# Optimization experiments

Hardware: AMD Instinct MI355X
Metric: run time of the kernel (lower is better)

The kernel has to match this reference:

```python
import math
import jax, jax.numpy as jnp
import numpy as np

B, S, H, NH, BS, R = 2, 4096, 1024, 16, 64, 3
HD = H // NH          # 64 head dim
L = S // BS           # 64 blocks
PEN = -10000.0


def _make_rand_attn():
    # data-independent random block plan (like HF bigbird, seeded numpy),
    # per head, per middle query block: R random key blocks excluding
    # global blocks (0, L-1) and the sliding window (i-1, i, i+1)
    rng = np.random.RandomState(42)
    ra = np.zeros((NH, L - 2, R), dtype=np.int64)
    for h in range(NH):
        for i in range(1, L - 1):
            choices = np.array([j for j in range(L) if j not in (0, i - 1, i, i + 1, L - 1)])
            ra[h, i - 1] = rng.choice(choices, R, replace=False)
    return ra


def setup_inputs():
    key = jax.random.key(0)
    ks = jax.random.split(key, 8)
    sc = 1.0 / math.sqrt(H)
    return {
        "Q": jax.random.normal(ks[0], (B, S, H), jnp.float32),
        "K": jax.random.normal(ks[1], (B, S, H), jnp.float32),
        "V": jax.random.normal(ks[2], (B, S, H), jnp.float32),
        "mask": jnp.ones((B, S), jnp.float32),
        "Wq": jax.random.normal(ks[3], (H, H), jnp.float32) * sc,
        "bq": jnp.zeros((H,), jnp.float32),
        "Wk": jax.random.normal(ks[4], (H, H), jnp.float32) * sc,
        "bk": jnp.zeros((H,), jnp.float32),
        "Wv": jax.random.normal(ks[5], (H, H), jnp.float32) * sc,
        "bv": jnp.zeros((H,), jnp.float32),
        "rand_attn": jnp.asarray(_make_rand_attn()),
    }


def _forward(Q, K, V, mask, Wq, bq, Wk, bk, Wv, bv, rand_attn):
    rsd = 1.0 / math.sqrt(HD)
    sm = lambda x: jax.nn.softmax(x, axis=-1)

    def proj(x, W, b):  # torch Linear: x @ W^T + b, then split heads
        return (x @ W.T + b).reshape(B, S, NH, HD).transpose(0, 2, 1, 3)

    q = proj(Q, Wq, bq)  # [B,NH,S,HD]
    k = proj(K, Wk, bk)
    v = proj(V, Wv, bv)
    qb = q.reshape(B, NH, L, BS, HD)
    kb = k.reshape(B, NH, L, BS, HD)
    vb = v.reshape(B, NH, L, BS, HD)

    # ---- masks (derived from padding mask, as in HF create_masks_...) ----
    blocked = mask.reshape(B, L, BS)
    from_mask = mask[:, None, :, None]   # [B,1,S,1]
    to_mask = mask[:, None, None, :]     # [B,1,1,S]
    exp_to = jnp.concatenate([blocked[:, 1:-3], blocked[:, 2:-2], blocked[:, 3:-1]], axis=2)  # [B,L-4,3BS]
    band_mask = jnp.einsum('blq,blk->blqk', blocked[:, 2:-2], exp_to)[:, None]  # [B,1,L-4,BS,3BS]

    ra = jnp.broadcast_to(rand_attn[None], (B, NH, L - 2, R))
    bidx = jnp.arange(B)[:, None, None, None]
    hidx = jnp.arange(NH)[None, :, None, None]
    gk = kb[bidx, hidx, ra].reshape(B, NH, L - 2, R * BS, HD)  # gathered random key blocks
    gv = vb[bidx, hidx, ra].reshape(B, NH, L - 2, R * BS, HD)
    rm = blocked[bidx, ra].reshape(B, NH, L - 2, R * BS)
    rand_mask = jnp.einsum('blq,bhlk->bhlqk', blocked[:, 1:-1], rm)  # [B,NH,L-2,BS,R*BS]

    # ---- first block: dense attention over all keys ----
    p1 = jnp.einsum('bhqd,bhkd->bhqk', qb[:, :, 0], k) * rsd + (1.0 - to_mask) * PEN
    ctx_first = jnp.einsum('bhqk,bhkd->bhqd', sm(p1), v)

    # ---- second block: global(0) + window(1,2) + last + random ----
    k2 = jnp.concatenate([kb[:, :, 0], kb[:, :, 1], kb[:, :, 2], kb[:, :, -1], gk[:, :, 0]], axis=2)
    v2 = jnp.concatenate([vb[:, :, 0], vb[:, :, 1], vb[:, :, 2], vb[:, :, -1], gv[:, :, 0]], axis=2)
    p2 = jnp.einsum('bhqd,bhkd->bhqk', qb[:, :, 1], k2) * rsd
    seq_pad2 = jnp.concatenate([to_mask[..., :3 * BS], to_mask[..., -BS:],
                                jnp.ones((B, 1, 1, R * BS), mask.dtype)], axis=3)
    rand_pad2 = jnp.concatenate([jnp.ones((B, NH, BS, 4 * BS), mask.dtype), rand_mask[:, :, 0]], axis=3)
    p2 = p2 + (1.0 - jnp.minimum(seq_pad2, rand_pad2)) * PEN
    ctx_second = jnp.einsum('bhqk,bhkd->bhqd', sm(p2), v2)

    # ---- middle blocks: band (3 sliding) + random + 2 global ----
    exp_k = jnp.concatenate([kb[:, :, 1:-3], kb[:, :, 2:-2], kb[:, :, 3:-1]], axis=3)  # [B,NH,L-4,3BS,HD]
    exp_v = jnp.concatenate([vb[:, :, 1:-3], vb[:, :, 2:-2], vb[:, :, 3:-1]], axis=3)
    mq = qb[:, :, 2:-2]
    inner = jnp.einsum('bhlqd,bhlkd->bhlqk', mq, exp_k) * rsd + (1.0 - band_mask) * PEN
    randp = jnp.einsum('bhlqd,bhlkd->bhlqk', mq, gk[:, :, 1:-1]) * rsd + (1.0 - rand_mask[:, :, 1:-1]) * PEN
    firstp = jnp.einsum('bhlqd,bhkd->bhlqk', mq, kb[:, :, 0]) * rsd + (1.0 - to_mask[:, :, :, None, :BS]) * PEN
    lastp = jnp.einsum('bhlqd,bhkd->bhlqk', mq, kb[:, :, -1]) * rsd + (1.0 - to_mask[:, :, :, None, -BS:]) * PEN
    w = sm(jnp.concatenate([firstp, inner, randp, lastp], axis=-1))  # [B,NH,L-4,BS,(5+R)*BS]
    ctx_mid = jnp.einsum('bhlqk,bhlkd->bhlqd', w[..., BS:4 * BS], exp_v)
    ctx_mid += jnp.einsum('bhlqk,bhlkd->bhlqd', w[..., 4 * BS:(4 + R) * BS], gv[:, :, 1:-1])
    ctx_mid += jnp.einsum('bhlqk,bhkd->bhlqd', w[..., :BS], vb[:, :, 0])
    ctx_mid += jnp.einsum('bhlqk,bhkd->bhlqd', w[..., -BS:], vb[:, :, -1])

    # ---- second-to-last block ----
    k3 = jnp.concatenate([kb[:, :, 0], kb[:, :, -3], kb[:, :, -2], kb[:, :, -1], gk[:, :, -1]], axis=2)
    v3 = jnp.concatenate([vb[:, :, 0], vb[:, :, -3], vb[:, :, -2], vb[:, :, -1], gv[:, :, -1]], axis=2)
    p3 = jnp.einsum('bhqd,bhkd->bhqk', qb[:, :, -2], k3) * rsd
    seq_pad3 = jnp.concatenate([to_mask[..., :BS], to_mask[..., -3 * BS:],
                                jnp.ones((B, 1, 1, R * BS), mask.dtype)], axis=3)
    rand_pad3 = jnp.concatenate([jnp.ones((B, NH, BS, 4 * BS), mask.dtype), rand_mask[:, :, -1]], axis=3)
    p3 = p3 + (1.0 - jnp.minimum(seq_pad3, rand_pad3)) * PEN
    ctx_seclast = jnp.einsum('bhqk,bhkd->bhqd', sm(p3), v3)

    # ---- last block: dense attention over all keys ----
    p4 = jnp.einsum('bhqd,bhkd->bhqk', qb[:, :, -1], k) * rsd + (1.0 - to_mask) * PEN
    ctx_last = jnp.einsum('bhqk,bhkd->bhqd', sm(p4), v)

    ctx = jnp.concatenate([ctx_first[:, :, None], ctx_second[:, :, None], ctx_mid,
                           ctx_seclast[:, :, None], ctx_last[:, :, None]], axis=2)
    ctx = ctx.reshape(B, NH, S, HD) * from_mask
    return ctx.transpose(0, 2, 1, 3).reshape(B, S, NH * HD)


def reference(Q, K, V, mask, Wq, bq, Wk, bk, Wv, bv, rand_attn):
    return _forward(Q, K, V, mask, Wq, bq, Wk, bk, Wv, bv, rand_attn)
```

## Files before the change

### kernel.cpp

```cpp
#include <hip/hip_runtime.h>
#include <hip/hip_bf16.h>
#include <stdint.h>

#define BB 2
#define SS 4096
#define HH 1024
#define NHh 16
#define HD 64
#define LL 64
#define BS 64
#define RR 3
#define PENf (-10000.0f)
#define L2E 1.44269504f
#define PENL (-14426.9504f)

typedef unsigned int uint;
typedef __attribute__((ext_vector_type(8))) short bf16x8;
typedef __attribute__((ext_vector_type(4))) float f32x4;

__device__ __forceinline__ ushort f2bf(float f) {
    union { float f; uint u; } v; v.f = f;
    uint u = v.u;
    return (ushort)((u + 0x7fffu + ((u >> 16) & 1u)) >> 16);
}
__device__ __forceinline__ uint pack_bf(float a, float b) {
    uint r;
    asm("v_cvt_pk_bf16_f32 %0, %1, %2" : "=v"(r) : "v"(a), "v"(b));
    return r;
}
__device__ __forceinline__ float fexp2(float x) {
    float r;
    asm("v_exp_f32 %0, %1" : "=v"(r) : "v"(x));
    return r;
}
__device__ __forceinline__ float fmax3(float a, float b, float c) {
    float r;
    asm("v_max3_f32 %0, %1, %2, %3" : "=v"(r) : "v"(a), "v"(b), "v"(c));
    return r;
}
__device__ __forceinline__ uint scale_pair(uint w) {
    float lo = __uint_as_float(w << 16) * 0.125f;
    float hi = __uint_as_float(w & 0xffff0000u) * 0.125f;
    return pack_bf(lo, hi);
}
__device__ __forceinline__ uint4 scale4(uint4 w) {
    uint4 o;
    o.x = scale_pair(w.x); o.y = scale_pair(w.y);
    o.z = scale_pair(w.z); o.w = scale_pair(w.w);
    return o;
}
__device__ __forceinline__ void async16(const ushort* g, ushort* l) {
    __builtin_amdgcn_global_load_lds((const __attribute__((address_space(1))) uint*)g,
                                     (__attribute__((address_space(3))) uint*)l,
                                     16, 0, 0);
}

__global__ __launch_bounds__(256)
void cvt_kernel(const float* __restrict__ Xq, const float* __restrict__ Xk,
                const float* __restrict__ Xv, const float* __restrict__ Wq,
                const float* __restrict__ Wk, const float* __restrict__ Wv,
                ushort* __restrict__ Xbf, ushort* __restrict__ Wbf)
{
    const size_t XTOT = (size_t)3 * BB * SS * HH;
    const uint u = blockIdx.x * 256 + threadIdx.x;
    const size_t e = (size_t)u * 8;
    const float* src; ushort* dst;
    if (e < XTOT) {
        const int zz = (int)(e >> 23);
        src = (zz == 0 ? Xq : zz == 1 ? Xk : Xv) + (e & ((1u << 23) - 1));
        dst = Xbf + e;
    } else {
        const size_t e2 = e - XTOT;
        const int zz = (int)(e2 >> 20);
        src = (zz == 0 ? Wq : zz == 1 ? Wk : Wv) + (e2 & ((1u << 20) - 1));
        dst = Wbf + e2;
    }
    float4 a = ((const float4*)src)[0];
    float4 c = ((const float4*)src)[1];
    uint4 o;
    o.x = pack_bf(a.x, a.y); o.y = pack_bf(a.z, a.w);
    o.z = pack_bf(c.x, c.y); o.w = pack_bf(c.z, c.w);
    *(uint4*)dst = o;
}

__global__ __launch_bounds__(512)
void gemm6_kernel(const ushort* __restrict__ Xbf, const ushort* __restrict__ Wbf,
                  const float* __restrict__ bq, const float* __restrict__ bk,
                  const float* __restrict__ bv,
                  ushort* __restrict__ qb, ushort* __restrict__ kb,
                  ushort* __restrict__ vbT)
{
    __shared__ __align__(16) ushort smem6[36864];

    const int z = blockIdx.z;
    const ushort* Ag = Xbf + (size_t)z * ((size_t)BB * SS * HH);
    const ushort* Bg = Wbf + (size_t)z * (HH * HH);
    const float* bias = (z == 0) ? bq : (z == 1) ? bk : bv;
    const bool zv = (z == 2);

    const int tid = threadIdx.x;
    const int m0 = blockIdx.x * 128;
    const int n0 = blockIdx.y * 256;
    const int wave = tid >> 6;
    const int lane = tid & 63;
    const int l15 = lane & 15;
    const int quad = lane >> 4;
    const int wr = wave >> 2;
    const int wc = wave & 3;

    f32x4 acc[4][4];
#pragma unroll
    for (int i = 0; i < 4; ++i)
#pragma unroll
        for (int j = 0; j < 4; ++j) acc[i][j] = (f32x4){0.f, 0.f, 0.f, 0.f};

    const int trow = tid >> 2;
    const int tcol = ((tid & 3) ^ ((tid >> 3) & 3)) * 8;
    const ushort* Ath  = Ag + (size_t)(m0 + trow) * HH + tcol;
    const ushort* Bth  = Bg + (size_t)(n0 + trow) * HH + tcol;
    const ushort* Bth2 = Bth + (size_t)128 * HH;
    const int sl8 = (quad ^ ((l15 >> 1) & 3)) * 8;

#define STAGE6(kt_, bb_)                                               \
    do {                                                               \
        const int k0_ = (kt_) * 32;                                    \
        const int sb_ = (bb_) * 12288 + wave * 512;                    \
        async16(Ath + k0_,  smem6 + sb_);                              \
        async16(Bth + k0_,  smem6 + sb_ + 4096);                       \
        async16(Bth2 + k0_, smem6 + sb_ + 8192);                       \
    } while (0)

#define TB6(kt_, bpi_, VM_, DOSTAGE_, sbf_)                                         \
    do {                                                                            \
        const int bo_ = (bpi_) * 12288;                                             \
        asm volatile("s_waitcnt vmcnt(" #VM_ ")" ::: "memory");                     \
        __builtin_amdgcn_s_barrier();                                               \
        __builtin_amdgcn_sched_barrier(0);                                          \
        const ushort* Ab_ = smem6 + bo_;                                            \
        const ushort* Bb_ = smem6 + bo_ + 4096;                                     \
        bf16x8 af_[4], bf_[4];                                                      \
        _Pragma("unroll")                                                           \
        for (int mt = 0; mt < 4; ++mt)                                              \
            af_[mt] = *(const bf16x8*)(Ab_ + (wr * 64 + mt * 16 + l15) * 32 + sl8); \
        _Pragma("unroll")                                                           \
        for (int nt = 0; nt < 4; ++nt)                                              \
            bf_[nt] = *(const bf16x8*)(Bb_ + (wc * 64 + nt * 16 + l15) * 32 + sl8); \
        if (DOSTAGE_) STAGE6((kt_) + 2, sbf_);                                      \
        __builtin_amdgcn_s_setprio(1);                                              \
        if (zv) {                                                                   \
            _Pragma("unroll")                                                       \
            for (int i = 0; i < 4; ++i)                                             \
                _Pragma("unroll")                                                   \
                for (int j = 0; j < 4; ++j)                                         \
                    acc[i][j] = __builtin_amdgcn_mfma_f32_16x16x32_bf16(            \
                        af_[i], bf_[j], acc[i][j], 0, 0, 0);                        \
        } else {                                                                    \
            _Pragma("unroll")                                                       \
            for (int i = 0; i < 4; ++i)                                             \
                _Pragma("unroll")                                                   \
                for (int j = 0; j < 4; ++j)                                         \
                    acc[i][j] = __builtin_amdgcn_mfma_f32_16x16x32_bf16(            \
                        bf_[i], af_[j], acc[i][j], 0, 0, 0);                        \
        }                                                                           \
        __builtin_amdgcn_s_setprio(0);                                              \
    } while (0)

    STAGE6(0, 0); STAGE6(1, 1);

    for (int k3 = 0; k3 < 30; k3 += 3) {
        TB6(k3 + 0, 0, 3, 1, 2);
        TB6(k3 + 1, 1, 3, 1, 0);
        TB6(k3 + 2, 2, 3, 1, 1);
    }
    TB6(30, 0, 3, 0, 0);
    TB6(31, 1, 0, 0, 0);
#undef TB6
#undef STAGE6

    if (!zv) {
        ushort* outp = (z == 0) ? qb : kb;
#pragma unroll
        for (int wt = 0; wt < 4; ++wt) {
            const int nb = n0 + wc * 64 + wt * 16 + quad * 4;
            const float4 b4 = *(const float4*)&bias[nb];
            const int nh = nb >> 6;
            const int hd = nb & 63;
#pragma unroll
            for (int xt = 0; xt < 4; ++xt) {
                const int m = m0 + wr * 64 + xt * 16 + l15;
                const int bgl = m >> 12, s = m & 4095;
                uint2 pk;
                pk.x = pack_bf(acc[wt][xt][0] + b4.x, acc[wt][xt][1] + b4.y);
                pk.y = pack_bf(acc[wt][xt][2] + b4.z, acc[wt][xt][3] + b4.w);
                *(uint2*)&outp[((size_t)((bgl << 4) | nh) * SS + s) * HD + hd] = pk;
            }
        }
    } else {
        __syncthreads();
        ushort* stg = smem6;
        const int bgl = m0 >> 12;
#pragma unroll
        for (int nt = 0; nt < 4; ++nt) {
            const int n_local = wc * 64 + nt * 16 + l15;
            const float bn = bias[n0 + n_local];
#pragma unroll
            for (int mt = 0; mt < 4; ++mt) {
                const int m_base = wr * 64 + mt * 16 + quad * 4;
                uint2 pk;
                pk.x = pack_bf(acc[mt][nt][0] + bn, acc[mt][nt][1] + bn);
                pk.y = pack_bf(acc[mt][nt][2] + bn, acc[mt][nt][3] + bn);
                *(uint2*)(stg + n_local * 136 + m_base) = pk;
            }
        }
        __syncthreads();
        const int n_row = tid >> 1;
        const int half = tid & 1;
        const int n = n0 + n_row;
        const int nh = n >> 6, hd = n & 63;
        const uint4* src = (const uint4*)(stg + n_row * 136 + half * 64);
        uint4* dst = (uint4*)(vbT + ((size_t)((bgl << 4) | nh) * HD + hd) * SS
                              + (m0 & 4095) + half * 64);
#pragma unroll
        for (int jj = 0; jj < 8; ++jj) dst[jj] = src[jj];
    }
}

__global__ __launch_bounds__(256)
void proj3_kernel(const float* __restrict__ Xq, const float* __restrict__ Xk,
                  const float* __restrict__ Xv,
                  const float* __restrict__ Wq, const float* __restrict__ Wk,
                  const float* __restrict__ Wv,
                  const float* __restrict__ bq, const float* __restrict__ bk,
                  const float* __restrict__ bv,
                  ushort* __restrict__ qb, ushort* __restrict__ kb,
                  ushort* __restrict__ vbT)
{
    __shared__ __align__(16) ushort smem[128 * 136];
    ushort* As = smem;
    ushort* Bs = smem + 128 * 40;

    const int z = blockIdx.z;
    const float* X    = (z == 0) ? Xq : (z == 1) ? Xk : Xv;
    const float* W    = (z == 0) ? Wq : (z == 1) ? Wk : Wv;
    const float* bias = (z == 0) ? bq : (z == 1) ? bk : bv;

    const int tid = threadIdx.x;
    const int m0 = blockIdx.x * 128;
    const int n0 = blockIdx.y * 128;
    const int wave = tid >> 6;
    const int lane = tid & 63;
    const int l15 = lane & 15;
    const int quad = lane >> 4;
    const int wr = wave >> 1, wc = wave & 1;

    f32x4 acc[4][4];
#pragma unroll
    for (int mt = 0; mt < 4; ++mt)
#pragma unroll
        for (int nt = 0; nt < 4; ++nt) acc[mt][nt] = (f32x4){0.f, 0.f, 0.f, 0.f};

    const int srow = tid >> 1;
    const int shalf = tid & 1;
    const float* xp = X + (size_t)(m0 + srow) * HH + shalf * 16;
    const float* wp = W + (size_t)(n0 + srow) * HH + shalf * 16;
    ushort* asw = As + srow * 40 + shalf * 16;
    ushort* bsw = Bs + srow * 40 + shalf * 16;

    for (int k0 = 0; k0 < HH; k0 += 32) {
        float4 a0 = *(const float4*)(xp + k0);
        float4 a1 = *(const float4*)(xp + k0 + 4);
        float4 a2 = *(const float4*)(xp + k0 + 8);
        float4 a3 = *(const float4*)(xp + k0 + 12);
        float4 b0 = *(const float4*)(wp + k0);
        float4 b1 = *(const float4*)(wp + k0 + 4);
        float4 b2 = *(const float4*)(wp + k0 + 8);
        float4 b3 = *(const float4*)(wp + k0 + 12);
        __syncthreads();
        uint4 pa, pb;
        pa.x = pack_bf(a0.x, a0.y); pa.y = pack_bf(a0.z, a0.w);
        pa.z = pack_bf(a1.x, a1.y); pa.w = pack_bf(a1.z, a1.w);
        *(uint4*)asw = pa;
        pa.x = pack_bf(a2.x, a2.y); pa.y = pack_bf(a2.z, a2.w);
        pa.z = pack_bf(a3.x, a3.y); pa.w = pack_bf(a3.z, a3.w);
        *(uint4*)(asw + 8) = pa;
        pb.x = pack_bf(b0.x, b0.y); pb.y = pack_bf(b0.z, b0.w);
        pb.z = pack_bf(b1.x, b1.y); pb.w = pack_bf(b1.z, b1.w);
        *(uint4*)bsw = pb;
        pb.x = pack_bf(b2.x, b2.y); pb.y = pack_bf(b2.z, b2.w);
        pb.z = pack_bf(b3.x, b3.y); pb.w = pack_bf(b3.z, b3.w);
        *(uint4*)(bsw + 8) = pb;
        __syncthreads();

        bf16x8 af[4], bfr[4];
#pragma unroll
        for (int mt = 0; mt < 4; ++mt)
            af[mt] = *(const bf16x8*)(As + (wr * 64 + mt * 16 + l15) * 40 + quad * 8);
#pragma unroll
        for (int nt = 0; nt < 4; ++nt)
            bfr[nt] = *(const bf16x8*)(Bs + (wc * 64 + nt * 16 + l15) * 40 + quad * 8);
#pragma unroll
        for (int mt = 0; mt < 4; ++mt)
#pragma unroll
            for (int nt = 0; nt < 4; ++nt)
                acc[mt][nt] = __builtin_amdgcn_mfma_f32_16x16x32_bf16(af[mt], bfr[nt], acc[mt][nt], 0, 0, 0);
    }

    if (z < 2) {
        ushort* outp = (z == 0) ? qb : kb;
#pragma unroll
        for (int nt = 0; nt < 4; ++nt) {
            const int n = n0 + wc * 64 + nt * 16 + l15;
            const float bn = bias[n];
            const int nh = n >> 6, hd = n & 63;
#pragma unroll
            for (int mt = 0; mt < 4; ++mt) {
#pragma unroll
                for (int rr = 0; rr < 4; ++rr) {
                    const int m = m0 + wr * 64 + mt * 16 + quad * 4 + rr;
                    const int bgl = m >> 12, s = m & 4095;
                    outp[((size_t)((bgl << 4) | nh) * SS + s) * HD + hd] = f2bf(acc[mt][nt][rr] + bn);
                }
            }
        }
    } else {
        __syncthreads();
        ushort* stg = smem;
#pragma unroll
        for (int nt = 0; nt < 4; ++nt) {
            const int n_local = wc * 64 + nt * 16 + l15;
            const float bn = bias[n0 + n_local];
#pragma unroll
            for (int mt = 0; mt < 4; ++mt) {
                const int m_base = wr * 64 + mt * 16 + quad * 4;
                uint2 pk;
                pk.x = pack_bf(acc[mt][nt][0] + bn, acc[mt][nt][1] + bn);
                pk.y = pack_bf(acc[mt][nt][2] + bn, acc[mt][nt][3] + bn);
                *(uint2*)(stg + n_local * 136 + m_base) = pk;
            }
        }
        __syncthreads();
        const int n_row = tid >> 1;
        const int half = tid & 1;
        const int n = n0 + n_row;
        const int nh = n >> 6, hd = n & 63;
        const int bgl = m0 >> 12;
        const int sbase = (m0 & 4095) + half * 64;
        const uint4* src = (const uint4*)(stg + n_row * 136 + half * 64);
        uint4* dst = (uint4*)(vbT + ((size_t)((bgl << 4) | nh) * HD + hd) * SS + sbase);
#pragma unroll
        for (int j = 0; j < 8; ++j) dst[j] = src[j];
    }
}

__global__ __launch_bounds__(256)
void attn_kernel(const ushort* __restrict__ qg, const ushort* __restrict__ kg,
                 const ushort* __restrict__ vTg,
                 const float* __restrict__ mask, const int* __restrict__ rand_attn,
                 float* __restrict__ out, float* __restrict__ partO,
                 float* __restrict__ partML)
{
    __shared__ __align__(16) ushort qs_ps[64][72];
    __shared__ __align__(16) ushort ks2[2][2][64][32];
    __shared__ __align__(16) ushort vs2[2][2][64][32];
    __shared__ __align__(16) float qm_s[64];
    __shared__ __align__(16) float km_s[2][64];

    const int tid = threadIdx.x;
    const int wid = blockIdx.x;
    const int bh = wid / 78;
    const int r = wid - bh * 78;
    const int b = bh >> 4, h = bh & 15;

    int i, nkb;
    int kbl[8], pfl[8];
    bool dense;
    int part = 0, which = 0;
    if (r < 62) {
        dense = false;
        i = r + 1;
        const int* ra = rand_attn + ((size_t)h * (LL - 2) + (i - 1)) * RR;
        if (i == 1) {
            kbl[0] = 0; kbl[1] = 1; kbl[2] = 2; kbl[3] = LL - 1;
            kbl[4] = ra[0]; kbl[5] = ra[1]; kbl[6] = ra[2]; kbl[7] = 0;
            pfl[0] = pfl[1] = pfl[2] = pfl[3] = 0;
            pfl[4] = pfl[5] = pfl[6] = 1; pfl[7] = 0;
            nkb = 7;
        } else if (i == LL - 2) {
            kbl[0] = 0; kbl[1] = LL - 3; kbl[2] = LL - 2; kbl[3] = LL - 1;
            kbl[4] = ra[0]; kbl[5] = ra[1]; kbl[6] = ra[2]; kbl[7] = 0;
            pfl[0] = pfl[1] = pfl[2] = pfl[3] = 0;
            pfl[4] = pfl[5] = pfl[6] = 1; pfl[7] = 0;
            nkb = 7;
        } else {
            kbl[0] = 0;      pfl[0] = 0;
            kbl[1] = i - 1;  pfl[1] = 1;
            kbl[2] = i;      pfl[2] = 1;
            kbl[3] = i + 1;  pfl[3] = 1;
            kbl[4] = LL - 1; pfl[4] = 0;
            kbl[5] = ra[0]; kbl[6] = ra[1]; kbl[7] = ra[2];
            pfl[5] = pfl[6] = pfl[7] = 1;
            nkb = 8;
        }
    } else {
        dense = true;
        const int r2 = r - 62;
        which = r2 >> 3;
        part = r2 & 7;
        i = which ? (LL - 1) : 0;
        nkb = 8;
#pragma unroll
        for (int j = 0; j < 8; ++j) { kbl[j] = part * 8 + j; pfl[j] = 0; }
    }

    const int lane = tid & 63;
    const int wave = tid >> 6;
    const int l15 = lane & 15;
    const int quad = lane >> 4;
    const int srow = lane >> 2;
    const int p8s = (((lane & 3) ^ ((srow >> 1) & 3))) * 8;
    const ushort* kgb = kg + (size_t)bh * SS * HD;
    const ushort* vgb = vTg + (size_t)bh * HD * SS;
    const ushort* kl = kgb + (size_t)(wave * 16 + srow) * HD + p8s;
    const ushort* vl = vgb + (size_t)(wave * 16 + srow) * SS + p8s;
    const float* maskb = mask + (size_t)b * SS;

#define STAGE_KV(kb_, bp)                                                \
    do {                                                                 \
        const ushort* ka_ = kl + ((size_t)(kb_) << 12);                  \
        async16(ka_,      &ks2[bp][0][wave * 16][0]);                    \
        async16(ka_ + 32, &ks2[bp][1][wave * 16][0]);                    \
        const ushort* va_ = vl + ((uint)(kb_) << 6);                     \
        async16(va_,      &vs2[bp][0][wave * 16][0]);                    \
        async16(va_ + 32, &vs2[bp][1][wave * 16][0]);                    \
    } while (0)

    {
        const int row = tid >> 2;
        const int c0 = (tid & 3) * 16;
        const ushort* src = qg + ((size_t)bh * SS + i * BS + row) * HD + c0;
        uint4 w0 = *(const uint4*)src;
        uint4 w1 = *(const uint4*)(src + 8);
        *(uint4*)&qs_ps[row][c0] = scale4(w0);
        *(uint4*)&qs_ps[row][c0 + 8] = scale4(w1);
        if (tid < 64) qm_s[tid] = maskb[i * BS + tid];
    }
    STAGE_KV(kbl[0], 0);
    if (tid < 64) km_s[0][tid] = maskb[kbl[0] * BS + tid];
    __syncthreads();

    bf16x8 aq[2];
    aq[0] = *(const bf16x8*)&qs_ps[wave * 16 + l15][quad * 8];
    aq[1] = *(const bf16x8*)&qs_ps[wave * 16 + l15][32 + quad * 8];
    const float qm = qm_s[wave * 16 + l15];
// ... 128 lines not shown

__global__ __launch_bounds__(64)
void combine_kernel(const float* __restrict__ partO, const float* __restrict__ partML,
                    const float* __restrict__ mask, float* __restrict__ out)
{
    const int g4 = blockIdx.x;
    const int g = g4 >> 2;
    const int bh = g >> 1, which = g & 1;
    const int b = bh >> 4, h = bh & 15;
    const int i = which ? (LL - 1) : 0;
    const int t = threadIdx.x;
    const int row = ((g4 & 3) << 4) | (t >> 2);
    const int d0 = (t & 3) * 16;
    const int base = g * 8;

    float mp[8], lp[8];
    float M = -1e30f;
#pragma unroll
    for (int p = 0; p < 8; ++p) {
        mp[p] = partML[(base + p) * 128 + row];
        lp[p] = partML[(base + p) * 128 + 64 + row];
        M = fmaxf(M, mp[p]);
    }
    float L = 0.0f, w[8];
#pragma unroll
    for (int p = 0; p < 8; ++p) { w[p] = fexp2(mp[p] - M); L += lp[p] * w[p]; }

    float4 o[4];
#pragma unroll
    for (int j = 0; j < 4; ++j) o[j] = make_float4(0.f, 0.f, 0.f, 0.f);
#pragma unroll
    for (int p = 0; p < 8; ++p) {
        const float* po = partO + (size_t)(base + p) * 4096 + row * 64 + d0;
#pragma unroll
        for (int j = 0; j < 4; ++j) {
            float4 v = *(const float4*)(po + j * 4);
            o[j].x = fmaf(w[p], v.x, o[j].x);
            o[j].y = fmaf(w[p], v.y, o[j].y);
            o[j].z = fmaf(w[p], v.z, o[j].z);
            o[j].w = fmaf(w[p], v.w, o[j].w);
        }
    }
    const float fm = mask[(size_t)b * SS + i * BS + row];
    const float inv = fm / L;
    float* dst = out + ((size_t)b * SS + i * BS + row) * HH + h * HD + d0;
#pragma unroll
    for (int j = 0; j < 4; ++j) {
        float4 v;
        v.x = o[j].x * inv; v.y = o[j].y * inv;
        v.z = o[j].z * inv; v.w = o[j].w * inv;
        *(float4*)(dst + j * 4) = v;
    }
}

extern "C" void kernel_launch(void* const* d_in, const int* in_sizes, int n_in,
                              void* d_out, int out_size, void* d_ws, size_t ws_size,
                              hipStream_t stream) {
    (void)in_sizes; (void)n_in; (void)out_size;
    const float* Q    = (const float*)d_in[0];
    const float* K    = (const float*)d_in[1];
    const float* V    = (const float*)d_in[2];
    const float* mask = (const float*)d_in[3];
    const float* Wq   = (const float*)d_in[4];
    const float* bq   = (const float*)d_in[5];
    const float* Wk   = (const float*)d_in[6];
    const float* bk   = (const float*)d_in[7];
    const float* Wv   = (const float*)d_in[8];
    const float* bv   = (const float*)d_in[9];
    const int*   ra   = (const int*)d_in[10];
    float* out = (float*)d_out;

    const size_t qkv = (size_t)BB * NHh * SS * HD;
    ushort* qb  = (ushort*)d_ws;
    ushort* kb  = qb + qkv;
    ushort* vbT = kb + qkv;
    float* partO  = (float*)(vbT + qkv);
    float* partML = partO + (size_t)512 * 4096;
    ushort* Xbf = (ushort*)(partML + (size_t)512 * 128);
    ushort* Wbf = Xbf + 3 * qkv;
    const size_t need = (size_t)((char*)(Wbf + (size_t)3 * HH * HH) - (char*)d_ws);

    if (ws_size >= need) {
        cvt_kernel<<<13824, 256, 0, stream>>>(Q, K, V, Wq, Wk, Wv, Xbf, Wbf);
        gemm6_kernel<<<dim3(64, 4, 3), 512, 0, stream>>>(Xbf, Wbf, bq, bk, bv, qb, kb, vbT);
    } else {
        proj3_kernel<<<dim3(64, 8, 3), 256, 0, stream>>>(Q, K, V, Wq, Wk, Wv, bq, bk, bv,
                                                         qb, kb, vbT);
    }
    attn_kernel<<<dim3(BB * NHh * 78), 256, 0, stream>>>(qb, kb, vbT, mask, ra,
                                                         out, partO, partML);
    combine_kernel<<<dim3(BB * NHh * 2 * 4), 64, 0, stream>>>(partO, partML, mask, out);
}
```

Measured before the change: 292.8 us.

## Enlarge QKV projection GEMM tile to 256x256 with K=64 double-buffered stages

The projection GEMM moves from 128x256 output tiles with K=32 triple-buffered stages to 256x256 tiles with K=64 double-buffered stages, using 128 KB of LDS. Each wave now accumulates an 8x4 grid of MFMA tiles, and A/B prefetch is split and interleaved with the compute phases. This raises arithmetic intensity per LDS and global load and halves the block count. In exchange it uses more registers and LDS, launches only 384 blocks, and waits on vmcnt(0) every iteration, which weakens pipelining. The V-transpose epilogue is redone in two passes to fit the staging layout.

Measured after the change: 459.0 us. 56.8% more time.

```diff
diff --git a/kernel.cpp b/kernel.cpp
--- a/kernel.cpp
+++ b/kernel.cpp
@@ -84,13 +84,13 @@
 }
 
 __global__ __launch_bounds__(512)
-void gemm6_kernel(const ushort* __restrict__ Xbf, const ushort* __restrict__ Wbf,
+void gemmL_kernel(const ushort* __restrict__ Xbf, const ushort* __restrict__ Wbf,
                   const float* __restrict__ bq, const float* __restrict__ bk,
                   const float* __restrict__ bv,
                   ushort* __restrict__ qb, ushort* __restrict__ kb,
                   ushort* __restrict__ vbT)
 {
-    __shared__ __align__(16) ushort smem6[36864];
+    __shared__ __align__(16) ushort smemL[65536];
 
     const int z = blockIdx.z;
     const ushort* Ag = Xbf + (size_t)z * ((size_t)BB * SS * HH);
@@ -99,7 +99,7 @@
     const bool zv = (z == 2);
 
     const int tid = threadIdx.x;
-    const int m0 = blockIdx.x * 128;
+    const int m0 = blockIdx.x * 256;
     const int n0 = blockIdx.y * 256;
     const int wave = tid >> 6;
     const int lane = tid & 63;
@@ -108,120 +108,192 @@
     const int wr = wave >> 2;
     const int wc = wave & 3;
 
-    f32x4 acc[4][4];
-#pragma unroll
-    for (int i = 0; i < 4; ++i)
-#pragma unroll
-        for (int j = 0; j < 4; ++j) acc[i][j] = (f32x4){0.f, 0.f, 0.f, 0.f};
-
-    const int trow = tid >> 2;
-    const int tcol = ((tid & 3) ^ ((tid >> 3) & 3)) * 8;
-    const ushort* Ath  = Ag + (size_t)(m0 + trow) * HH + tcol;
-    const ushort* Bth  = Bg + (size_t)(n0 + trow) * HH + tcol;
-    const ushort* Bth2 = Bth + (size_t)128 * HH;
-    const int sl8 = (quad ^ ((l15 >> 1) & 3)) * 8;
-
-#define STAGE6(kt_, bb_)                                               \
+    f32x4 acc[8][4];
+#pragma unroll
+    for (int mi = 0; mi < 8; ++mi)
+#pragma unroll
+        for (int ni = 0; ni < 4; ++ni) acc[mi][ni] = (f32x4){0.f, 0.f, 0.f, 0.f};
+
+    const int srow8 = lane >> 3;
+    const int sslot = (lane & 7) ^ srow8;
+    const ushort* AsrcB = Ag + (size_t)(m0 + wave * 32 + srow8) * HH + sslot * 8;
+    const ushort* BsrcB = Bg + (size_t)(n0 + wave * 32 + srow8) * HH + sslot * 8;
+
+    const int rs0 = (quad ^ (l15 & 7)) * 8;
+    const int rs1 = ((4 + quad) ^ (l15 & 7)) * 8;
+    const int arow = (wr * 128 + l15) * 64;
+    const int brow = (wc * 64 + l15) * 64;
+
+#define STAGE_LA(kt_, bb_)                                             \
     do {                                                               \
-        const int k0_ = (kt_) * 32;                                    \
-        const int sb_ = (bb_) * 12288 + wave * 512;                    \
-        async16(Ath + k0_,  smem6 + sb_);                              \
-        async16(Bth + k0_,  smem6 + sb_ + 4096);                       \
-        async16(Bth2 + k0_, smem6 + sb_ + 8192);                       \
+        const ushort* sa_ = AsrcB + (kt_) * 64;                        \
+        ushort* da_ = smemL + (bb_) * 32768 + wave * 2048;             \
+        async16(sa_,           da_);                                   \
+        async16(sa_ + 8 * HH,  da_ + 512);                             \
+        async16(sa_ + 16 * HH, da_ + 1024);                            \
+        async16(sa_ + 24 * HH, da_ + 1536);                            \
     } while (0)
-
-#define TB6(kt_, bpi_, VM_, DOSTAGE_, sbf_)                                         \
-    do {                                                                            \
-        const int bo_ = (bpi_) * 12288;                                             \
-        asm volatile("s_waitcnt vmcnt(" #VM_ ")" ::: "memory");                     \
-        __builtin_amdgcn_s_barrier();                                               \
-        __builtin_amdgcn_sched_barrier(0);                                          \
-        const ushort* Ab_ = smem6 + bo_;                                            \
-        const ushort* Bb_ = smem6 + bo_ + 4096;                                     \
-        bf16x8 af_[4], bf_[4];                                                      \
-        _Pragma("unroll")                                                           \
-        for (int mt = 0; mt < 4; ++mt)                                              \
-            af_[mt] = *(const bf16x8*)(Ab_ + (wr * 64 + mt * 16 + l15) * 32 + sl8); \
-        _Pragma("unroll")                                                           \
-        for (int nt = 0; nt < 4; ++nt)                                              \
-            bf_[nt] = *(const bf16x8*)(Bb_ + (wc * 64 + nt * 16 + l15) * 32 + sl8); \
-        if (DOSTAGE_) STAGE6((kt_) + 2, sbf_);                                      \
-        __builtin_amdgcn_s_setprio(1);                                              \
-        if (zv) {                                                                   \
-            _Pragma("unroll")                                                       \
-            for (int i = 0; i < 4; ++i)                                             \
-                _Pragma("unroll")                                                   \
-                for (int j = 0; j < 4; ++j)                                         \
-                    acc[i][j] = __builtin_amdgcn_mfma_f32_16x16x32_bf16(            \
-                        af_[i], bf_[j], acc[i][j], 0, 0, 0);                        \
-        } else {                                                                    \
-            _Pragma("unroll")                                                       \
-            for (int i = 0; i < 4; ++i)                                             \
-                _Pragma("unroll")                                                   \
-                for (int j = 0; j < 4; ++j)                                         \
-                    acc[i][j] = __builtin_amdgcn_mfma_f32_16x16x32_bf16(            \
-                        bf_[i], af_[j], acc[i][j], 0, 0, 0);                        \
-        }                                                                           \
-        __builtin_amdgcn_s_setprio(0);                                              \
+#define STAGE_LB(kt_, bb_)                                             \
+    do {                                                               \
+        const ushort* sb2_ = BsrcB + (kt_) * 64;                       \
+        ushort* db_ = smemL + (bb_) * 32768 + 16384 + wave * 2048;     \
+        async16(sb2_,           db_);                                  \
+        async16(sb2_ + 8 * HH,  db_ + 512);                            \
+        async16(sb2_ + 16 * HH, db_ + 1024);                           \
+        async16(sb2_ + 24 * HH, db_ + 1536);                           \
     } while (0)
 
-    STAGE6(0, 0); STAGE6(1, 1);
-
-    for (int k3 = 0; k3 < 30; k3 += 3) {
-        TB6(k3 + 0, 0, 3, 1, 2);
-        TB6(k3 + 1, 1, 3, 1, 0);
-        TB6(k3 + 2, 2, 3, 1, 1);
-    }
-    TB6(30, 0, 3, 0, 0);
-    TB6(31, 1, 0, 0, 0);
-#undef TB6
-#undef STAGE6
+    STAGE_LA(0, 0); STAGE_LB(0, 0);
+
+    for (int kt = 0; kt < 16; ++kt) {
+        const int cur = kt & 1;
+        asm volatile("s_waitcnt vmcnt(0)" ::: "memory");
+        __builtin_amdgcn_s_barrier();
+        __builtin_amdgcn_sched_barrier(0);
+        const ushort* Ab = smemL + cur * 32768;
+        const ushort* Bb = Ab + 16384;
+        bf16x8 afr[8], bq0, bq1;
+
+        if (kt + 1 < 16) STAGE_LA(kt + 1, cur ^ 1);
+#pragma unroll
+        for (int mi = 0; mi < 8; ++mi)
+            afr[mi] = *(const bf16x8*)(Ab + arow + mi * 1024 + rs0);
+        bq0 = *(const bf16x8*)(Bb + brow + rs0);
+        bq1 = *(const bf16x8*)(Bb + brow + 1024 + rs0);
+        __builtin_amdgcn_s_setprio(1);
+        if (zv) {
+#pragma unroll
+            for (int mi = 0; mi < 8; ++mi) {
+                acc[mi][0] = __builtin_amdgcn_mfma_f32_16x16x32_bf16(afr[mi], bq0, acc[mi][0], 0, 0, 0);
+                acc[mi][1] = __builtin_amdgcn_mfma_f32_16x16x32_bf16(afr[mi], bq1, acc[mi][1], 0, 0, 0);
+            }
+        } else {
+#pragma unroll
+            for (int mi = 0; mi < 8; ++mi) {
+                acc[mi][0] = __builtin_amdgcn_mfma_f32_16x16x32_bf16(bq0, afr[mi], acc[mi][0], 0, 0, 0);
+                acc[mi][1] = __builtin_amdgcn_mfma_f32_16x16x32_bf16(bq1, afr[mi], acc[mi][1], 0, 0, 0);
+            }
+        }
+        __builtin_amdgcn_s_setprio(0);
+        __builtin_amdgcn_sched_barrier(0);
+
+        if (kt + 1 < 16) STAGE_LB(kt + 1, cur ^ 1);
+        bq0 = *(const bf16x8*)(Bb + brow + 2048 + rs0);
+        bq1 = *(const bf16x8*)(Bb + brow + 3072 + rs0);
+        __builtin_amdgcn_s_setprio(1);
+        if (zv) {
+#pragma unroll
+            for (int mi = 0; mi < 8; ++mi) {
+                acc[mi][2] = __builtin_amdgcn_mfma_f32_16x16x32_bf16(afr[mi], bq0, acc[mi][2], 0, 0, 0);
+                acc[mi][3] = __builtin_amdgcn_mfma_f32_16x16x32_bf16(afr[mi], bq1, acc[mi][3], 0, 0, 0);
+            }
+        } else {
+#pragma unroll
+            for (int mi = 0; mi < 8; ++mi) {
+                acc[mi][2] = __builtin_amdgcn_mfma_f32_16x16x32_bf16(bq0, afr[mi], acc[mi][2], 0, 0, 0);
+                acc[mi][3] = __builtin_amdgcn_mfma_f32_16x16x32_bf16(bq1, afr[mi], acc[mi][3], 0, 0, 0);
+            }
+        }
+        __builtin_amdgcn_s_setprio(0);
+        __builtin_amdgcn_sched_barrier(0);
+
+#pragma unroll
+        for (int mi = 0; mi < 8; ++mi)
+            afr[mi] = *(const bf16x8*)(Ab + arow + mi * 1024 + rs1);
+        bq0 = *(const bf16x8*)(Bb + brow + rs1);
+        bq1 = *(const bf16x8*)(Bb + brow + 1024 + rs1);
+        __builtin_amdgcn_s_setprio(1);
+        if (zv) {
+#pragma unroll
+            for (int mi = 0; mi < 8; ++mi) {
+                acc[mi][0] = __builtin_amdgcn_mfma_f32_16x16x32_bf16(afr[mi], bq0, acc[mi][0], 0, 0, 0);
+                acc[mi][1] = __builtin_amdgcn_mfma_f32_16x16x32_bf16(afr[mi], bq1, acc[mi][1], 0, 0, 0);
+            }
+        } else {
+#pragma unroll
+            for (int mi = 0; mi < 8; ++mi) {
+                acc[mi][0] = __builtin_amdgcn_mfma_f32_16x16x32_bf16(bq0, afr[mi], acc[mi][0], 0, 0, 0);
+                acc[mi][1] = __builtin_amdgcn_mfma_f32_16x16x32_bf16(bq1, afr[mi], acc[mi][1], 0, 0, 0);
+            }
+        }
+        __builtin_amdgcn_s_setprio(0);
+        __builtin_amdgcn_sched_barrier(0);
+
+        bq0 = *(const bf16x8*)(Bb + brow + 2048 + rs1);
+        bq1 = *(const bf16x8*)(Bb + brow + 3072 + rs1);
+        __builtin_amdgcn_s_setprio(1);
+        if (zv) {
+#pragma unroll
+            for (int mi = 0; mi < 8; ++mi) {
+                acc[mi][2] = __builtin_amdgcn_mfma_f32_16x16x32_bf16(afr[mi], bq0, acc[mi][2], 0, 0, 0);
+                acc[mi][3] = __builtin_amdgcn_mfma_f32_16x16x32_bf16(afr[mi], bq1, acc[mi][3], 0, 0, 0);
+            }
+        } else {
+#pragma unroll
+            for (int mi = 0; mi < 8; ++mi) {
+                acc[mi][2] = __builtin_amdgcn_mfma_f32_16x16x32_bf16(bq0, afr[mi], acc[mi][2], 0, 0, 0);
+                acc[mi][3] = __builtin_amdgcn_mfma_f32_16x16x32_bf16(bq1, afr[mi], acc[mi][3], 0, 0, 0);
+            }
+        }
+        __builtin_amdgcn_s_setprio(0);
+        __builtin_amdgcn_sched_barrier(0);
+    }
+#undef STAGE_LA
+#undef STAGE_LB
 
     if (!zv) {
         ushort* outp = (z == 0) ? qb : kb;
 #pragma unroll
-        for (int wt = 0; wt < 4; ++wt) {
-            const int nb = n0 + wc * 64 + wt * 16 + quad * 4;
+        for (int ni = 0; ni < 4; ++ni) {
+            const int nb = n0 + wc * 64 + ni * 16 + quad * 4;
             const float4 b4 = *(const float4*)&bias[nb];
             const int nh = nb >> 6;
             const int hd = nb & 63;
 #pragma unroll
-            for (int xt = 0; xt < 4; ++xt) {
-                const int m = m0 + wr * 64 + xt * 16 + l15;
+            for (int mi = 0; mi < 8; ++mi) {
+                const int m = m0 + wr * 128 + mi * 16 + l15;
                 const int bgl = m >> 12, s = m & 4095;
                 uint2 pk;
-                pk.x = pack_bf(acc[wt][xt][0] + b4.x, acc[wt][xt][1] + b4.y);
-                pk.y = pack_bf(acc[wt][xt][2] + b4.z, acc[wt][xt][3] + b4.w);
+                pk.x = pack_bf(acc[mi][ni][0] + b4.x, acc[mi][ni][1] + b4.y);
+                pk.y = pack_bf(acc[mi][ni][2] + b4.z, acc[mi][ni][3] + b4.w);
                 *(uint2*)&outp[((size_t)((bgl << 4) | nh) * SS + s) * HD + hd] = pk;
             }
         }
     } else {
         __syncthreads();
-        ushort* stg = smem6;
+        ushort* stg = smemL;
         const int bgl = m0 >> 12;
 #pragma unroll
-        for (int nt = 0; nt < 4; ++nt) {
-            const int n_local = wc * 64 + nt * 16 + l15;
-            const float bn = bias[n0 + n_local];
-#pragma unroll
-            for (int mt = 0; mt < 4; ++mt) {
-                const int m_base = wr * 64 + mt * 16 + quad * 4;
-                uint2 pk;
-                pk.x = pack_bf(acc[mt][nt][0] + bn, acc[mt][nt][1] + bn);
-                pk.y = pack_bf(acc[mt][nt][2] + bn, acc[mt][nt][3] + bn);
-                *(uint2*)(stg + n_local * 136 + m_base) = pk;
-            }
-        }
-        __syncthreads();
-        const int n_row = tid >> 1;
-        const int half = tid & 1;
-        const int n = n0 + n_row;
-        const int nh = n >> 6, hd = n & 63;
-        const uint4* src = (const uint4*)(stg + n_row * 136 + half * 64);
-        uint4* dst = (uint4*)(vbT + ((size_t)((bgl << 4) | nh) * HD + hd) * SS
-                              + (m0 & 4095) + half * 64);
-#pragma unroll
-        for (int jj = 0; jj < 8; ++jj) dst[jj] = src[jj];
+        for (int p = 0; p < 2; ++p) {
+            __syncthreads();
+            if ((wc >> 1) == p) {
+#pragma unroll
+                for (int ni = 0; ni < 4; ++ni) {
+                    const int nl = (wc & 1) * 64 + ni * 16 + l15;
+                    const float bn = bias[n0 + p * 128 + nl];
+#pragma unroll
+                    for (int mi = 0; mi < 8; ++mi) {
+                        const int mb = wr * 128 + mi * 16 + quad * 4;
+                        uint2 pk;
+                        pk.x = pack_bf(acc[mi][ni][0] + bn, acc[mi][ni][1] + bn);
+                        pk.y = pack_bf(acc[mi][ni][2] + bn, acc[mi][ni][3] + bn);
+                        *(uint2*)(stg + nl * 272 + mb) = pk;
+                    }
+                }
+            }
+            __syncthreads();
+            {
+                const int row = tid >> 2;
+                const int seg = tid & 3;
+                const int n = n0 + p * 128 + row;
+                const int nh = n >> 6, hd = n & 63;
+                const uint4* src = (const uint4*)(stg + row * 272 + seg * 64);
+                uint4* dst = (uint4*)(vbT + ((size_t)((bgl << 4) | nh) * HD + hd) * SS
+                                      + (m0 & 4095) + seg * 64);
+#pragma unroll
+                for (int jj = 0; jj < 8; ++jj) dst[jj] = src[jj];
+            }
+        }
     }
 }
 
@@ -663,7 +735,7 @@
 
     if (ws_size >= need) {
         cvt_kernel<<<13824, 256, 0, stream>>>(Q, K, V, Wq, Wk, Wv, Xbf, Wbf);
-        gemm6_kernel<<<dim3(64, 4, 3), 512, 0, stream>>>(Xbf, Wbf, bq, bk, bv, qb, kb, vbT);
+        gemmL_kernel<<<dim3(32, 4, 3), 512, 0, stream>>>(Xbf, Wbf, bq, bk, bv, qb, kb, vbT);
     } else {
         proj3_kernel<<<dim3(64, 8, 3), 256, 0, stream>>>(Q, K, V, Wq, Wk, Wv, bq, bk, bv,
                                                          qb, kb, vbT);
```

## Shrink projection GEMM tile to 128x128 and remap attention blocks for locality

Applied to the files above, without the earlier changes.

The QKV projection GEMM moves from 512-thread 128x256 tiles to 256-thread 128x128 tiles. Each wave now stages two 16-row chunks of A and B per k-step, and the vmcnt waits are adjusted to match. The grid doubles to 1536 blocks, which should improve occupancy and load balance across CUs at the cost of more global reads of X per output. The attention kernel's block index is also remapped so that 8 consecutive blocks map to different (batch, head) groups, to spread work across XCDs and caches.

New measurement: 289.9 us. No clear change (-1.0%).

```diff
diff --git a/kernel.cpp b/kernel.cpp
--- a/kernel.cpp
+++ b/kernel.cpp
@@ -83,14 +83,14 @@
     *(uint4*)dst = o;
 }
 
-__global__ __launch_bounds__(512)
-void gemm6_kernel(const ushort* __restrict__ Xbf, const ushort* __restrict__ Wbf,
-                  const float* __restrict__ bq, const float* __restrict__ bk,
-                  const float* __restrict__ bv,
-                  ushort* __restrict__ qb, ushort* __restrict__ kb,
-                  ushort* __restrict__ vbT)
+__global__ __launch_bounds__(256)
+void gemm2b_kernel(const ushort* __restrict__ Xbf, const ushort* __restrict__ Wbf,
+                   const float* __restrict__ bq, const float* __restrict__ bk,
+                   const float* __restrict__ bv,
+                   ushort* __restrict__ qb, ushort* __restrict__ kb,
+                   ushort* __restrict__ vbT)
 {
-    __shared__ __align__(16) ushort smem6[36864];
+    __shared__ __align__(16) ushort smem2[24576];
 
     const int z = blockIdx.z;
     const ushort* Ag = Xbf + (size_t)z * ((size_t)BB * SS * HH);
@@ -100,13 +100,12 @@
 
     const int tid = threadIdx.x;
     const int m0 = blockIdx.x * 128;
-    const int n0 = blockIdx.y * 256;
+    const int n0 = blockIdx.y * 128;
     const int wave = tid >> 6;
     const int lane = tid & 63;
     const int l15 = lane & 15;
     const int quad = lane >> 4;
-    const int wr = wave >> 2;
-    const int wc = wave & 3;
+    const int wr = wave >> 1, wc = wave & 1;
 
     f32x4 acc[4][4];
 #pragma unroll
@@ -114,30 +113,31 @@
 #pragma unroll
         for (int j = 0; j < 4; ++j) acc[i][j] = (f32x4){0.f, 0.f, 0.f, 0.f};
 
-    const int trow = tid >> 2;
-    const int tcol = ((tid & 3) ^ ((tid >> 3) & 3)) * 8;
-    const ushort* Ath  = Ag + (size_t)(m0 + trow) * HH + tcol;
-    const ushort* Bth  = Bg + (size_t)(n0 + trow) * HH + tcol;
-    const ushort* Bth2 = Bth + (size_t)128 * HH;
+    const int srow4 = lane >> 2;
+    const int sslot = ((lane & 3) ^ ((lane >> 3) & 3)) * 8;
+    const ushort* Ath = Ag + (size_t)(m0 + wave * 32 + srow4) * HH + sslot;
+    const ushort* Bth = Bg + (size_t)(n0 + wave * 32 + srow4) * HH + sslot;
     const int sl8 = (quad ^ ((l15 >> 1) & 3)) * 8;
 
-#define STAGE6(kt_, bb_)                                               \
+#define STAGE2(kt_, bb_)                                               \
     do {                                                               \
         const int k0_ = (kt_) * 32;                                    \
-        const int sb_ = (bb_) * 12288 + wave * 512;                    \
-        async16(Ath + k0_,  smem6 + sb_);                              \
-        async16(Bth + k0_,  smem6 + sb_ + 4096);                       \
-        async16(Bth2 + k0_, smem6 + sb_ + 8192);                       \
+        ushort* dA_ = smem2 + (bb_) * 8192 + wave * 1024;              \
+        ushort* dB_ = dA_ + 4096;                                      \
+        async16(Ath + k0_,           dA_);                             \
+        async16(Ath + 16 * HH + k0_, dA_ + 512);                       \
+        async16(Bth + k0_,           dB_);                             \
+        async16(Bth + 16 * HH + k0_, dB_ + 512);                       \
     } while (0)
 
-#define TB6(kt_, bpi_, VM_, DOSTAGE_, sbf_)                                         \
+#define TB2(kt_, bpi_, VM_, DOSTAGE_, sbf_)                                         \
     do {                                                                            \
-        const int bo_ = (bpi_) * 12288;                                             \
+        const int bo_ = (bpi_) * 8192;                                              \
         asm volatile("s_waitcnt vmcnt(" #VM_ ")" ::: "memory");                     \
         __builtin_amdgcn_s_barrier();                                               \
         __builtin_amdgcn_sched_barrier(0);                                          \
-        const ushort* Ab_ = smem6 + bo_;                                            \
-        const ushort* Bb_ = smem6 + bo_ + 4096;                                     \
+        const ushort* Ab_ = smem2 + bo_;                                            \
+        const ushort* Bb_ = smem2 + bo_ + 4096;                                     \
         bf16x8 af_[4], bf_[4];                                                      \
         _Pragma("unroll")                                                           \
         for (int mt = 0; mt < 4; ++mt)                                              \
@@ -145,7 +145,7 @@
         _Pragma("unroll")                                                           \
         for (int nt = 0; nt < 4; ++nt)                                              \
             bf_[nt] = *(const bf16x8*)(Bb_ + (wc * 64 + nt * 16 + l15) * 32 + sl8); \
-        if (DOSTAGE_) STAGE6((kt_) + 2, sbf_);                                      \
+        if (DOSTAGE_) STAGE2((kt_) + 2, sbf_);                                      \
         __builtin_amdgcn_s_setprio(1);                                              \
         if (zv) {                                                                   \
             _Pragma("unroll")                                                       \
@@ -165,17 +165,17 @@
         __builtin_amdgcn_s_setprio(0);                                              \
     } while (0)
 
-    STAGE6(0, 0); STAGE6(1, 1);
+    STAGE2(0, 0); STAGE2(1, 1);
 
     for (int k3 = 0; k3 < 30; k3 += 3) {
-        TB6(k3 + 0, 0, 3, 1, 2);
-        TB6(k3 + 1, 1, 3, 1, 0);
-        TB6(k3 + 2, 2, 3, 1, 1);
-    }
-    TB6(30, 0, 3, 0, 0);
-    TB6(31, 1, 0, 0, 0);
-#undef TB6
-#undef STAGE6
+        TB2(k3 + 0, 0, 4, 1, 2);
+        TB2(k3 + 1, 1, 4, 1, 0);
+        TB2(k3 + 2, 2, 4, 1, 1);
+    }
+    TB2(30, 0, 4, 0, 0);
+    TB2(31, 1, 0, 0, 0);
+#undef TB2
+#undef STAGE2
 
     if (!zv) {
         ushort* outp = (z == 0) ? qb : kb;
@@ -197,7 +197,7 @@
         }
     } else {
         __syncthreads();
-        ushort* stg = smem6;
+        ushort* stg = smem2;
         const int bgl = m0 >> 12;
 #pragma unroll
         for (int nt = 0; nt < 4; ++nt) {
@@ -217,11 +217,11 @@
         const int half = tid & 1;
         const int n = n0 + n_row;
         const int nh = n >> 6, hd = n & 63;
+        const int sbase = (m0 & 4095) + half * 64;
         const uint4* src = (const uint4*)(stg + n_row * 136 + half * 64);
-        uint4* dst = (uint4*)(vbT + ((size_t)((bgl << 4) | nh) * HD + hd) * SS
-                              + (m0 & 4095) + half * 64);
-#pragma unroll
-        for (int jj = 0; jj < 8; ++jj) dst[jj] = src[jj];
+        uint4* dst = (uint4*)(vbT + ((size_t)((bgl << 4) | nh) * HD + hd) * SS + sbase);
+#pragma unroll
+        for (int j = 0; j < 8; ++j) dst[j] = src[j];
     }
 }
 
@@ -366,9 +366,12 @@
     __shared__ __align__(16) float km_s[2][64];
 
     const int tid = threadIdx.x;
-    const int wid = blockIdx.x;
-    const int bh = wid / 78;
-    const int r = wid - bh * 78;
+    const int wid0 = blockIdx.x;
+    const int xg = wid0 & 7;
+    const int tg = wid0 >> 3;
+    const int jg = tg / 78;
+    const int r  = tg - jg * 78;
+    const int bh = xg * 4 + jg;
     const int b = bh >> 4, h = bh & 15;
 
     int i, nkb;
@@ -663,7 +666,7 @@
 
     if (ws_size >= need) {
         cvt_kernel<<<13824, 256, 0, stream>>>(Q, K, V, Wq, Wk, Wv, Xbf, Wbf);
-        gemm6_kernel<<<dim3(64, 4, 3), 512, 0, stream>>>(Xbf, Wbf, bq, bk, bv, qb, kb, vbT);
+        gemm2b_kernel<<<dim3(64, 8, 3), 256, 0, stream>>>(Xbf, Wbf, bq, bk, bv, qb, kb, vbT);
     } else {
         proj3_kernel<<<dim3(64, 8, 3), 256, 0, stream>>>(Q, K, V, Wq, Wk, Wv, bq, bk, bv,
                                                          qb, kb, vbT);
```

## Double GEMM K-tile to 64 with split staging and remap attention blocks

Applied to the files above, without the earlier changes.

The projection GEMM now stages 64-wide K tiles instead of 32, with an 8-slot XOR swizzle. The shared buffer doubles to 144KB and each tile runs as two 16-MFMA halves, with A and B loads interleaved between them. This halves the number of barriers and wait points per K step, at the cost of more LDS per block, which may limit occupancy. The attention kernel also remaps block IDs so consecutive workgroups cycle across 8 head groups, with the aim of spreading work and improving cache locality across XCDs.

Result: faster. 285.6 us (-2.5%).

```diff
diff --git a/kernel.cpp b/kernel.cpp
--- a/kernel.cpp
+++ b/kernel.cpp
@@ -84,13 +84,13 @@
 }
 
 __global__ __launch_bounds__(512)
-void gemm6_kernel(const ushort* __restrict__ Xbf, const ushort* __restrict__ Wbf,
-                  const float* __restrict__ bq, const float* __restrict__ bk,
-                  const float* __restrict__ bv,
-                  ushort* __restrict__ qb, ushort* __restrict__ kb,
-                  ushort* __restrict__ vbT)
+void gemm6v_kernel(const ushort* __restrict__ Xbf, const ushort* __restrict__ Wbf,
+                   const float* __restrict__ bq, const float* __restrict__ bk,
+                   const float* __restrict__ bv,
+                   ushort* __restrict__ qb, ushort* __restrict__ kb,
+                   ushort* __restrict__ vbT)
 {
-    __shared__ __align__(16) ushort smem6[36864];
+    __shared__ __align__(16) ushort smemV[73728];
 
     const int z = blockIdx.z;
     const ushort* Ag = Xbf + (size_t)z * ((size_t)BB * SS * HH);
@@ -114,38 +114,32 @@
 #pragma unroll
         for (int j = 0; j < 4; ++j) acc[i][j] = (f32x4){0.f, 0.f, 0.f, 0.f};
 
-    const int trow = tid >> 2;
-    const int tcol = ((tid & 3) ^ ((tid >> 3) & 3)) * 8;
-    const ushort* Ath  = Ag + (size_t)(m0 + trow) * HH + tcol;
-    const ushort* Bth  = Bg + (size_t)(n0 + trow) * HH + tcol;
-    const ushort* Bth2 = Bth + (size_t)128 * HH;
-    const int sl8 = (quad ^ ((l15 >> 1) & 3)) * 8;
-
-#define STAGE6(kt_, bb_)                                               \
+    const int trowV = tid >> 3;
+    const int sslotV = ((tid & 7) ^ (trowV & 7)) * 8;
+    const ushort* AthV = Ag + (size_t)(m0 + trowV) * HH + sslotV;
+    const ushort* BthV = Bg + (size_t)(n0 + trowV) * HH + sslotV;
+    const int rs0 = ((quad) ^ (l15 & 7)) * 8;
+    const int rs1 = ((4 + quad) ^ (l15 & 7)) * 8;
+
+#define STAGE_A(kt_, bb_)                                              \
     do {                                                               \
-        const int k0_ = (kt_) * 32;                                    \
-        const int sb_ = (bb_) * 12288 + wave * 512;                    \
-        async16(Ath + k0_,  smem6 + sb_);                              \
-        async16(Bth + k0_,  smem6 + sb_ + 4096);                       \
-        async16(Bth2 + k0_, smem6 + sb_ + 8192);                       \
+        const ushort* sa_ = AthV + (kt_) * 64;                         \
+        ushort* da_ = smemV + (bb_) * 24576 + wave * 512;              \
+        async16(sa_,           da_);                                   \
+        async16(sa_ + 64 * HH, da_ + 4096);                            \
     } while (0)
-
-#define TB6(kt_, bpi_, VM_, DOSTAGE_, sbf_)                                         \
+#define STAGE_B(kt_, bb_)                                              \
+    do {                                                               \
+        const ushort* sb_ = BthV + (kt_) * 64;                         \
+        ushort* db_ = smemV + (bb_) * 24576 + 8192 + wave * 512;       \
+        async16(sb_,            db_);                                  \
+        async16(sb_ + 64 * HH,  db_ + 4096);                           \
+        async16(sb_ + 128 * HH, db_ + 8192);                           \
+        async16(sb_ + 192 * HH, db_ + 12288);                          \
+    } while (0)
+
+#define MFMA16()                                                                    \
     do {                                                                            \
-        const int bo_ = (bpi_) * 12288;                                             \
-        asm volatile("s_waitcnt vmcnt(" #VM_ ")" ::: "memory");                     \
-        __builtin_amdgcn_s_barrier();                                               \
-        __builtin_amdgcn_sched_barrier(0);                                          \
-        const ushort* Ab_ = smem6 + bo_;                                            \
-        const ushort* Bb_ = smem6 + bo_ + 4096;                                     \
-        bf16x8 af_[4], bf_[4];                                                      \
-        _Pragma("unroll")                                                           \
-        for (int mt = 0; mt < 4; ++mt)                                              \
-            af_[mt] = *(const bf16x8*)(Ab_ + (wr * 64 + mt * 16 + l15) * 32 + sl8); \
-        _Pragma("unroll")                                                           \
-        for (int nt = 0; nt < 4; ++nt)                                              \
-            bf_[nt] = *(const bf16x8*)(Bb_ + (wc * 64 + nt * 16 + l15) * 32 + sl8); \
-        if (DOSTAGE_) STAGE6((kt_) + 2, sbf_);                                      \
         __builtin_amdgcn_s_setprio(1);                                              \
         if (zv) {                                                                   \
             _Pragma("unroll")                                                       \
@@ -165,17 +159,49 @@
         __builtin_amdgcn_s_setprio(0);                                              \
     } while (0)
 
-    STAGE6(0, 0); STAGE6(1, 1);
-
-    for (int k3 = 0; k3 < 30; k3 += 3) {
-        TB6(k3 + 0, 0, 3, 1, 2);
-        TB6(k3 + 1, 1, 3, 1, 0);
-        TB6(k3 + 2, 2, 3, 1, 1);
-    }
-    TB6(30, 0, 3, 0, 0);
-    TB6(31, 1, 0, 0, 0);
-#undef TB6
-#undef STAGE6
+#define TBV(kt_, bpi_, VM_, DSA_, DSB_, sbf_)                                       \
+    do {                                                                            \
+        asm volatile("s_waitcnt vmcnt(" #VM_ ")" ::: "memory");                     \
+        __builtin_amdgcn_s_barrier();                                               \
+        __builtin_amdgcn_sched_barrier(0);                                          \
+        const ushort* Ab_ = smemV + (bpi_) * 24576;                                 \
+        const ushort* Bb_ = Ab_ + 8192;                                             \
+        bf16x8 af_[4], bf_[4];                                                      \
+        _Pragma("unroll")                                                           \
+        for (int mt = 0; mt < 4; ++mt)                                              \
+            af_[mt] = *(const bf16x8*)(Ab_ + (wr * 64 + mt * 16 + l15) * 64 + rs0); \
+        _Pragma("unroll")                                                           \
+        for (int nt = 0; nt < 4; ++nt)                                              \
+            bf_[nt] = *(const bf16x8*)(Bb_ + (wc * 64 + nt * 16 + l15) * 64 + rs0); \
+        if (DSA_) STAGE_A((kt_) + 2, sbf_);                                         \
+        MFMA16();                                                                   \
+        __builtin_amdgcn_sched_barrier(0);                                          \
+        _Pragma("unroll")                                                           \
+        for (int mt = 0; mt < 4; ++mt)                                              \
+            af_[mt] = *(const bf16x8*)(Ab_ + (wr * 64 + mt * 16 + l15) * 64 + rs1); \
+        _Pragma("unroll")                                                           \
+        for (int nt = 0; nt < 4; ++nt)                                              \
+            bf_[nt] = *(const bf16x8*)(Bb_ + (wc * 64 + nt * 16 + l15) * 64 + rs1); \
+        if (DSB_) STAGE_B((kt_) + 2, sbf_);                                         \
+        MFMA16();                                                                   \
+    } while (0)
+
+    STAGE_A(0, 0); STAGE_B(0, 0);
+    STAGE_A(1, 1); STAGE_B(1, 1);
+
+    for (int k3 = 0; k3 < 12; k3 += 3) {
+        TBV(k3 + 0, 0, 6, 1, 1, 2);
+        TBV(k3 + 1, 1, 6, 1, 1, 0);
+        TBV(k3 + 2, 2, 6, 1, 1, 1);
+    }
+    TBV(12, 0, 6, 1, 1, 2);
+    TBV(13, 1, 6, 1, 1, 0);
+    TBV(14, 2, 6, 0, 0, 0);
+    TBV(15, 0, 0, 0, 0, 0);
+#undef TBV
+#undef MFMA16
+#undef STAGE_A
+#undef STAGE_B
 
     if (!zv) {
         ushort* outp = (z == 0) ? qb : kb;
@@ -197,7 +223,7 @@
         }
     } else {
         __syncthreads();
-        ushort* stg = smem6;
+        ushort* stg = smemV;
         const int bgl = m0 >> 12;
 #pragma unroll
         for (int nt = 0; nt < 4; ++nt) {
@@ -366,9 +392,12 @@
     __shared__ __align__(16) float km_s[2][64];
 
     const int tid = threadIdx.x;
-    const int wid = blockIdx.x;
-    const int bh = wid / 78;
-    const int r = wid - bh * 78;
+    const int wid0 = blockIdx.x;
+    const int xg = wid0 & 7;
+    const int tg = wid0 >> 3;
+    const int jg = tg / 78;
+    const int r  = tg - jg * 78;
+    const int bh = xg * 4 + jg;
     const int b = bh >> 4, h = bh & 15;
 
     int i, nkb;
@@ -663,7 +692,7 @@
 
     if (ws_size >= need) {
         cvt_kernel<<<13824, 256, 0, stream>>>(Q, K, V, Wq, Wk, Wv, Xbf, Wbf);
-        gemm6_kernel<<<dim3(64, 4, 3), 512, 0, stream>>>(Xbf, Wbf, bq, bk, bv, qb, kb, vbT);
+        gemm6v_kernel<<<dim3(64, 4, 3), 512, 0, stream>>>(Xbf, Wbf, bq, bk, bv, qb, kb, vbT);
     } else {
         proj3_kernel<<<dim3(64, 8, 3), 256, 0, stream>>>(Q, K, V, Wq, Wk, Wv, bq, bk, bv,
                                                          qb, kb, vbT);
```
